# Optimization experiments

Measured on AMD Instinct MI355X. Metric: run time of the kernel, lower is better.

The kernel has to match this reference:

```python
import jax, jax.numpy as jnp
import numpy as np

LEAKING_RATE = 0.5

def setup_inputs() -> dict:
    key = jax.random.key(0)
    k1, k2, k3 = jax.random.split(key, 3)
    B, T, I, R = 32, 4096, 64, 512
    x = jax.random.normal(k1, (B, T, I), dtype=jnp.float32)
    # input_projection weight ~ U(-1, 1), shape [R, I]
    w_in = jax.random.uniform(k2, (R, I), dtype=jnp.float32, minval=-1.0, maxval=1.0)
    # state_projection diagonal ~ U(-0.5, 0.5)
    d = jax.random.uniform(k3, (R,), dtype=jnp.float32, minval=-0.5, maxval=0.5)
    return {"x": x, "w_in": w_in, "d": d}

def reference(x, w_in, d):
    # Faithful to the original forward: the Python loop reads all_states[:, t, :],
    # which is ZERO at every step (never the previous state). Hence each timestep
    # is independent:
    #   state = 0
    #   new_state = tanh(d * state + x_t @ W_in^T) = tanh(x_t @ W_in^T)
    #   out_t = lr * state + (1 - lr) * new_state = (1 - lr) * tanh(x_t @ W_in^T)
    proj = jnp.einsum('bti,ri->btr', x, w_in)           # [B, T, R]
    zero_state = jnp.zeros_like(proj)
    new_state = jnp.tanh(zero_state * d + proj)
    out = LEAKING_RATE * zero_state + (1.0 - LEAKING_RATE) * new_state
    return out
```

## Files before the change

kernel.cpp:

```cpp
#include <hip/hip_runtime.h>

typedef int   i32x4 __attribute__((ext_vector_type(4)));
typedef float f32x4 __attribute__((ext_vector_type(4)));

#define M_ROWS 131072
#define N_COLS 512
#define K_DIM  64
#define MT     8
#define MAGIC  0x600DF00D
#define OPAD   516

#define MFMAI8 __builtin_amdgcn_mfma_i32_16x16x64_i8

__device__ __forceinline__ void lds_barrier() {
  asm volatile("s_waitcnt lgkmcnt(0)" ::: "memory");
  __builtin_amdgcn_s_barrier();
  __builtin_amdgcn_sched_barrier(0);
}

__device__ __forceinline__ float half_tanh_pre(float ps) {
  float t = __builtin_amdgcn_exp2f(ps);
  return 0.5f - __builtin_amdgcn_rcpf(t + 1.0f);
}

__device__ __forceinline__ void xquant16(const float* __restrict__ p,
                                         i32x4& hi, i32x4& lo) {
#pragma unroll
  for (int c = 0; c < 4; ++c) {
    f32x4 v = *(const f32x4*)(p + 4 * c);
    int a1 = 0, a0 = 0;
#pragma unroll
    for (int j = 0; j < 4; ++j) {
      float s = __builtin_rintf(v[j] * 2048.0f);
      s = fminf(fmaxf(s, -16319.f), 16319.f);
      const int q = (int)s;
      const int h = (q + 64) >> 7;
      const int l = q - (h << 7);
      a1 |= (h & 255) << (8 * j);
      a0 |= (l & 255) << (8 * j);
    }
    hi[c] = a1; lo[c] = a0;
  }
}

__global__ void probe_k(int* __restrict__ tab) {
  const int lane = threadIdx.x & 63;
  const int i16  = lane & 15;
  const int g    = lane >> 4;
  const i32x4 zi = {0, 0, 0, 0};

  int pig[4];
  bool ok = true;
  {
    const int bb = (g + 1) * 0x01010101;
    const i32x4 bgv = {bb, bb, bb, bb};
#pragma unroll
    for (int g0 = 0; g0 < 4; ++g0) {
      const int ab = (g == g0) ? 0x01010101 : 0;
      const i32x4 dA = {ab, ab, ab, ab};
      i32x4 dt = MFMAI8(dA, bgv, zi, 0, 0, 0);
      const int v = dt[0] >> 4;
      bool u = (dt[0] == (v << 4)) && (v >= 1) && (v <= 4);
#pragma unroll
      for (int q = 1; q < 4; ++q) u = u && (dt[q] == dt[0]);
      ok = ok && u;
      pig[g0] = v - 1;
    }
  }
  ok = ok && (((1 << pig[0]) | (1 << pig[1]) | (1 << pig[2]) | (1 << pig[3])) == 15);
  int pinv_g = 0;
#pragma unroll
  for (int g0 = 0; g0 < 4; ++g0) if (pig[g0] == g) pinv_g = g0;

  int rowv[4], colv[4];
  {
    const int vb = i16 * 0x01010101;
    const i32x4 vals  = {vb, vb, vb, vb};
    const i32x4 onesv = {0x01010101, 0x01010101, 0x01010101, 0x01010101};
    i32x4 d1 = MFMAI8(vals, onesv, zi, 0, 0, 0);
    i32x4 d2 = MFMAI8(onesv, vals, zi, 0, 0, 0);
#pragma unroll
    for (int q = 0; q < 4; ++q) {
      rowv[q] = d1[q] >> 6;
      colv[q] = d2[q] >> 6;
      ok = ok && (d1[q] == (rowv[q] << 6)) && (rowv[q] >= 0) && (rowv[q] < 16) &&
                 (d2[q] == (colv[q] << 6)) && (colv[q] >= 0) && (colv[q] < 16);
    }
  }

  {
    i32x4 ta, tb;
#pragma unroll
    for (int c = 0; c < 4; ++c) {
      int a = 0, b = 0;
#pragma unroll
      for (int j = 0; j < 4; ++j) {
        const int ka = 16 * g + 4 * c + j;
        const int kb = 16 * pinv_g + 4 * c + j;
        const int av = ((5 * i16 + 3 * ka) & 63) - 32;
        const int bv = ((7 * kb + 11 * i16) & 63) - 32;
        a |= (av & 255) << (8 * j);
        b |= (bv & 255) << (8 * j);
      }
      ta[c] = a; tb[c] = b;
    }
    i32x4 dt3 = MFMAI8(ta, tb, zi, 0, 0, 0);
#pragma unroll
    for (int q = 0; q < 4; ++q) {
      int ref = 0;
      for (int k = 0; k < 64; ++k)
        ref += (((5 * rowv[q] + 3 * k) & 63) - 32) * (((7 * k + 11 * colv[q]) & 63) - 32);
      ok = ok && (dt3[q] == ref);
    }
  }
  const bool all_ok = __all((int)ok);
  const bool vec = all_ok &&
      __all((int)(colv[0] == colv[1] && colv[1] == colv[2] && colv[2] == colv[3] &&
                  rowv[1] == rowv[0] + 1 && rowv[2] == rowv[0] + 2 &&
                  rowv[3] == rowv[0] + 3 && (rowv[0] & 3) == 0));

#pragma unroll
  for (int q = 0; q < 4; ++q) tab[lane * 4 + q] = (colv[q] << 8) | rowv[q];
  tab[256 + lane] = pinv_g;
  if (lane == 0) { tab[320] = all_ok ? MAGIC : 0; tab[321] = vec ? 1 : 0; }
}

__global__ __launch_bounds__(512, 4) void esn_m(const float* __restrict__ x,
                                                const float* __restrict__ w,
                                                const int* __restrict__ tab,
                                                float* __restrict__ out) {
  const int tid  = threadIdx.x;
  const int wv   = tid >> 6;
  const int lane = tid & 63;
  const int i16  = lane & 15;
  const int g    = lane >> 4;
  const int mb0  = blockIdx.x * (16 * MT);
  const i32x4 zi = {0, 0, 0, 0};

  __shared__ int   xq[MT][2][64][4];
  __shared__ float obuf[16 * OPAD];

  bool ok = false;
  int vecf = 0, pinv = 0;
  int rowv[4], colv[4];
  if (tab != nullptr) {
    const i32x4 rc = ((const i32x4*)tab)[lane];
#pragma unroll
    for (int q = 0; q < 4; ++q) { rowv[q] = rc[q] & 255; colv[q] = (rc[q] >> 8) & 255; }
    pinv = tab[256 + lane];
    ok   = (tab[320] == MAGIC);
    vecf = tab[321];
  }

  if (ok) {
    {
      i32x4 x1p, x0p;
      xquant16(x + (size_t)(mb0 + 16 * wv + i16) * K_DIM + 16 * pinv, x1p, x0p);
      *(i32x4*)&xq[wv][0][lane][0] = x1p;
      *(i32x4*)&xq[wv][1][lane][0] = x0p;
    }

    i32x4 w1p[4], w0p[4];
#pragma unroll
    for (int t = 0; t < 4; ++t) {
      const float* wb = w + (size_t)(64 * wv + 16 * t + i16) * K_DIM + 16 * g;
#pragma unroll
      for (int c = 0; c < 4; ++c) {
        f32x4 v = *(const f32x4*)(wb + 4 * c);
        int a1 = 0, a0 = 0;
#pragma unroll
        for (int j = 0; j < 4; ++j) {
          float s = __builtin_rintf(v[j] * 8192.0f);
          s = fminf(fmaxf(s, -8192.f), 8192.f);
          const int q = (int)s;
          const int h = (q + 64) >> 7;
          const int l = q - (h << 7);
          a1 |= (h & 255) << (8 * j);
          a0 |= (l & 255) << (8 * j);
        }
        w1p[t][c] = a1; w0p[t][c] = a0;
      }
    }
    __syncthreads();

    const float TANH_C = 2.8853900817779268f * 5.9604644775390625e-8f;
#pragma unroll 1
    for (int mi = 0; mi < MT; ++mi) {
      const int mb = mb0 + 16 * mi;
      const i32x4 x1p = *(const i32x4*)&xq[mi][0][lane][0];
      const i32x4 x0p = *(const i32x4*)&xq[mi][1][lane][0];

#pragma unroll
      for (int t = 0; t < 4; ++t) {
        i32x4 p11 = MFMAI8(w1p[t], x1p, zi, 0, 0, 0);
        i32x4 pm  = MFMAI8(w0p[t], x1p, zi, 0, 0, 0);
        pm        = MFMAI8(w1p[t], x0p, pm, 0, 0, 0);
        i32x4 p00 = MFMAI8(w0p[t], x0p, zi, 0, 0, 0);

        const int rb = 64 * wv + 16 * t;
        if (vecf) {
          f32x4 v;
#pragma unroll
          for (int q = 0; q < 4; ++q) {
            const float S = fmaf((float)p11[q], 16384.f,
                                 fmaf((float)pm[q], 128.f, (float)p00[q]));
            v[q] = half_tanh_pre(S * TANH_C);
          }
          *(f32x4*)&obuf[colv[0] * OPAD + rb + rowv[0]] = v;
        } else {
#pragma unroll
          for (int q = 0; q < 4; ++q) {
            const float S = fmaf((float)p11[q], 16384.f,
                                 fmaf((float)pm[q], 128.f, (float)p00[q]));
            obuf[colv[q] * OPAD + rb + rowv[q]] = half_tanh_pre(S * TANH_C);
          }
        }
      }
      lds_barrier();

#pragma unroll
      for (int p = 0; p < 4; ++p) {
        const int idx = p * 2048 + tid * 4;
        const int row = idx >> 9, col = idx & 511;
        const f32x4 v = *(const f32x4*)&obuf[row * OPAD + col];
        *(f32x4*)(out + (size_t)mb * N_COLS + idx) = v;
      }
      if (mi + 1 < MT) lds_barrier();
    }
  } else {
    const int r = tid;
    f32x4 wr[16];
    const f32x4* wp = (const f32x4*)(w + (size_t)r * K_DIM);
#pragma unroll
    for (int i = 0; i < 16; ++i) wr[i] = wp[i];

    const f32x4* xrow = (const f32x4*)(x + (size_t)mb0 * K_DIM);
    float* orow = out + (size_t)mb0 * N_COLS + r;
#pragma unroll 1
    for (int mi = 0; mi < 16 * MT; ++mi) {
      const f32x4* xr = xrow + (size_t)mi * 16;
      f32x4 acc = {0.f, 0.f, 0.f, 0.f};
#pragma unroll
      for (int kc = 0; kc < 16; kc += 4)
#pragma unroll
        for (int j = 0; j < 4; ++j) {
          acc[0] = fmaf(xr[kc + 0][j], wr[kc + 0][j], acc[0]);
          acc[1] = fmaf(xr[kc + 1][j], wr[kc + 1][j], acc[1]);
          acc[2] = fmaf(xr[kc + 2][j], wr[kc + 2][j], acc[2]);
          acc[3] = fmaf(xr[kc + 3][j], wr[kc + 3][j], acc[3]);
        }
      const float p = (acc[0] + acc[1]) + (acc[2] + acc[3]);
      orow[(size_t)mi * N_COLS] = half_tanh_pre(p * 2.8853900817779268f);
    }
  }
}

extern "C" void kernel_launch(void* const* d_in, const int* in_sizes, int n_in,
                              void* d_out, int out_size, void* d_ws, size_t ws_size,
                              hipStream_t stream) {
  const float* x = (const float*)d_in[0];
  const float* w = (const float*)d_in[1];
  float* out = (float*)d_out;

  int* tab = (ws_size >= 2048) ? (int*)d_ws : nullptr;
  if (tab) hipLaunchKernelGGL(probe_k, dim3(1), dim3(64), 0, stream, tab);

  dim3 grid(M_ROWS / (16 * MT));
  dim3 block(512);
  hipLaunchKernelGGL(esn_m, grid, block, 0, stream, x, w, tab, out);
}
```

Baseline: 74.99 us.

## Fuse MFMA layout probe into main kernel and double-buffer swizzled output tile

Moves the MFMA layout/correctness probe out of its separate launch and into the main kernel: wave 0 computes the table into shared memory while all waves quantize weights, which removes one kernel launch and its global round trip. The output staging buffer becomes double-buffered, so the trailing barrier at the end of each tile iteration can be dropped. Row padding is replaced by an XOR swizzle to avoid LDS bank conflicts. The cost is much more LDS per block (two full 16x512 fp32 tiles), which can lower the number of resident blocks per CU, and every block now repeats the probe work.

```diff
diff --git a/kernel.cpp b/kernel.cpp
--- a/kernel.cpp
+++ b/kernel.cpp
@@ -8,9 +8,12 @@
 #define K_DIM  64
 #define MT     8
 #define MAGIC  0x600DF00D
-#define OPAD   516
 
 #define MFMAI8 __builtin_amdgcn_mfma_i32_16x16x64_i8
+
+__device__ __forceinline__ int obuf_idx(int m, int r) {
+  return m * 512 + (r ^ ((m & 7) << 2));
+}
 
 __device__ __forceinline__ void lds_barrier() {
   asm volatile("s_waitcnt lgkmcnt(0)" ::: "memory");
@@ -43,92 +46,9 @@
   }
 }
 
-__global__ void probe_k(int* __restrict__ tab) {
-  const int lane = threadIdx.x & 63;
-  const int i16  = lane & 15;
-  const int g    = lane >> 4;
-  const i32x4 zi = {0, 0, 0, 0};
-
-  int pig[4];
-  bool ok = true;
-  {
-    const int bb = (g + 1) * 0x01010101;
-    const i32x4 bgv = {bb, bb, bb, bb};
-#pragma unroll
-    for (int g0 = 0; g0 < 4; ++g0) {
-      const int ab = (g == g0) ? 0x01010101 : 0;
-      const i32x4 dA = {ab, ab, ab, ab};
-      i32x4 dt = MFMAI8(dA, bgv, zi, 0, 0, 0);
-      const int v = dt[0] >> 4;
-      bool u = (dt[0] == (v << 4)) && (v >= 1) && (v <= 4);
-#pragma unroll
-      for (int q = 1; q < 4; ++q) u = u && (dt[q] == dt[0]);
-      ok = ok && u;
-      pig[g0] = v - 1;
-    }
-  }
-  ok = ok && (((1 << pig[0]) | (1 << pig[1]) | (1 << pig[2]) | (1 << pig[3])) == 15);
-  int pinv_g = 0;
-#pragma unroll
-  for (int g0 = 0; g0 < 4; ++g0) if (pig[g0] == g) pinv_g = g0;
-
-  int rowv[4], colv[4];
-  {
-    const int vb = i16 * 0x01010101;
-    const i32x4 vals  = {vb, vb, vb, vb};
-    const i32x4 onesv = {0x01010101, 0x01010101, 0x01010101, 0x01010101};
-    i32x4 d1 = MFMAI8(vals, onesv, zi, 0, 0, 0);
-    i32x4 d2 = MFMAI8(onesv, vals, zi, 0, 0, 0);
-#pragma unroll
-    for (int q = 0; q < 4; ++q) {
-      rowv[q] = d1[q] >> 6;
-      colv[q] = d2[q] >> 6;
-      ok = ok && (d1[q] == (rowv[q] << 6)) && (rowv[q] >= 0) && (rowv[q] < 16) &&
-                 (d2[q] == (colv[q] << 6)) && (colv[q] >= 0) && (colv[q] < 16);
-    }
-  }
-
-  {
-    i32x4 ta, tb;
-#pragma unroll
-    for (int c = 0; c < 4; ++c) {
-      int a = 0, b = 0;
-#pragma unroll
-      for (int j = 0; j < 4; ++j) {
-        const int ka = 16 * g + 4 * c + j;
-        const int kb = 16 * pinv_g + 4 * c + j;
-        const int av = ((5 * i16 + 3 * ka) & 63) - 32;
-        const int bv = ((7 * kb + 11 * i16) & 63) - 32;
-        a |= (av & 255) << (8 * j);
-        b |= (bv & 255) << (8 * j);
-      }
-      ta[c] = a; tb[c] = b;
-    }
-    i32x4 dt3 = MFMAI8(ta, tb, zi, 0, 0, 0);
-#pragma unroll
-    for (int q = 0; q < 4; ++q) {
-      int ref = 0;
-      for (int k = 0; k < 64; ++k)
-        ref += (((5 * rowv[q] + 3 * k) & 63) - 32) * (((7 * k + 11 * colv[q]) & 63) - 32);
-      ok = ok && (dt3[q] == ref);
-    }
-  }
-  const bool all_ok = __all((int)ok);
-  const bool vec = all_ok &&
-      __all((int)(colv[0] == colv[1] && colv[1] == colv[2] && colv[2] == colv[3] &&
-                  rowv[1] == rowv[0] + 1 && rowv[2] == rowv[0] + 2 &&
-                  rowv[3] == rowv[0] + 3 && (rowv[0] & 3) == 0));
-
-#pragma unroll
-  for (int q = 0; q < 4; ++q) tab[lane * 4 + q] = (colv[q] << 8) | rowv[q];
-  tab[256 + lane] = pinv_g;
-  if (lane == 0) { tab[320] = all_ok ? MAGIC : 0; tab[321] = vec ? 1 : 0; }
-}
-
-__global__ __launch_bounds__(512, 4) void esn_m(const float* __restrict__ x,
-                                                const float* __restrict__ w,
-                                                const int* __restrict__ tab,
-                                                float* __restrict__ out) {
+__global__ __launch_bounds__(512, 4) void esn_all(const float* __restrict__ x,
+                                                  const float* __restrict__ w,
+                                                  float* __restrict__ out) {
   const int tid  = threadIdx.x;
   const int wv   = tid >> 6;
   const int lane = tid & 63;
@@ -138,19 +58,121 @@
   const i32x4 zi = {0, 0, 0, 0};
 
   __shared__ int   xq[MT][2][64][4];
-  __shared__ float obuf[16 * OPAD];
-
-  bool ok = false;
-  int vecf = 0, pinv = 0;
+  __shared__ float obuf[2][16 * 512];
+
+  int* ptab = (int*)&obuf[0][0];
+
+  if (wv == 0) {
+    int pig[4];
+    bool ok = true;
+    {
+      const int bb = (g + 1) * 0x01010101;
+      const i32x4 bgv = {bb, bb, bb, bb};
+#pragma unroll
+      for (int g0 = 0; g0 < 4; ++g0) {
+        const int ab = (g == g0) ? 0x01010101 : 0;
+        const i32x4 dA = {ab, ab, ab, ab};
+        i32x4 dt = MFMAI8(dA, bgv, zi, 0, 0, 0);
+        const int v = dt[0] >> 4;
+        bool u = (dt[0] == (v << 4)) && (v >= 1) && (v <= 4);
+#pragma unroll
+        for (int q = 1; q < 4; ++q) u = u && (dt[q] == dt[0]);
+        ok = ok && u;
+        pig[g0] = v - 1;
+      }
+    }
+    ok = ok && (((1 << pig[0]) | (1 << pig[1]) | (1 << pig[2]) | (1 << pig[3])) == 15);
+    int pinv_g = 0;
+#pragma unroll
+    for (int g0 = 0; g0 < 4; ++g0) if (pig[g0] == g) pinv_g = g0;
+
+    int rowv[4], colv[4];
+    {
+      const int vb = i16 * 0x01010101;
+      const i32x4 vals  = {vb, vb, vb, vb};
+      const i32x4 onesv = {0x01010101, 0x01010101, 0x01010101, 0x01010101};
+      i32x4 d1 = MFMAI8(vals, onesv, zi, 0, 0, 0);
+      i32x4 d2 = MFMAI8(onesv, vals, zi, 0, 0, 0);
+#pragma unroll
+      for (int q = 0; q < 4; ++q) {
+        rowv[q] = d1[q] >> 6;
+        colv[q] = d2[q] >> 6;
+        ok = ok && (d1[q] == (rowv[q] << 6)) && (rowv[q] >= 0) && (rowv[q] < 16) &&
+                   (d2[q] == (colv[q] << 6)) && (colv[q] >= 0) && (colv[q] < 16);
+      }
+    }
+
+    {
+      i32x4 ta, tb;
+#pragma unroll
+      for (int c = 0; c < 4; ++c) {
+        int a = 0, b = 0;
+#pragma unroll
+        for (int j = 0; j < 4; ++j) {
+          const int ka = 16 * g + 4 * c + j;
+          const int kb = 16 * pinv_g + 4 * c + j;
+          const int av = ((5 * i16 + 3 * ka) & 63) - 32;
+          const int bv = ((7 * kb + 11 * i16) & 63) - 32;
+          a |= (av & 255) << (8 * j);
+          b |= (bv & 255) << (8 * j);
+        }
+        ta[c] = a; tb[c] = b;
+      }
+      i32x4 dt3 = MFMAI8(ta, tb, zi, 0, 0, 0);
+#pragma unroll
+      for (int q = 0; q < 4; ++q) {
+        int ref = 0;
+        for (int k = 0; k < 64; ++k)
+          ref += (((5 * rowv[q] + 3 * k) & 63) - 32) *
+                 (((7 * k + 11 * colv[q]) & 63) - 32);
+        ok = ok && (dt3[q] == ref);
+      }
+    }
+    const bool all_ok = __all((int)ok);
+    const bool vecw = all_ok &&
+        __all((int)(colv[0] == colv[1] && colv[1] == colv[2] && colv[2] == colv[3] &&
+                    rowv[1] == rowv[0] + 1 && rowv[2] == rowv[0] + 2 &&
+                    rowv[3] == rowv[0] + 3 && (rowv[0] & 3) == 0));
+
+#pragma unroll
+    for (int q = 0; q < 4; ++q) ptab[lane * 4 + q] = (colv[q] << 8) | rowv[q];
+    ptab[256 + lane] = pinv_g;
+    if (lane == 0) { ptab[320] = all_ok ? MAGIC : 0; ptab[321] = vecw ? 1 : 0; }
+  }
+
+  i32x4 w1p[4], w0p[4];
+#pragma unroll
+  for (int t = 0; t < 4; ++t) {
+    const float* wb = w + (size_t)(64 * wv + 16 * t + i16) * K_DIM + 16 * g;
+#pragma unroll
+    for (int c = 0; c < 4; ++c) {
+      f32x4 v = *(const f32x4*)(wb + 4 * c);
+      int a1 = 0, a0 = 0;
+#pragma unroll
+      for (int j = 0; j < 4; ++j) {
+        float s = __builtin_rintf(v[j] * 8192.0f);
+        s = fminf(fmaxf(s, -8192.f), 8192.f);
+        const int q = (int)s;
+        const int h = (q + 64) >> 7;
+        const int l = q - (h << 7);
+        a1 |= (h & 255) << (8 * j);
+        a0 |= (l & 255) << (8 * j);
+      }
+      w1p[t][c] = a1; w0p[t][c] = a0;
+    }
+  }
+
+  lds_barrier();
+
   int rowv[4], colv[4];
-  if (tab != nullptr) {
-    const i32x4 rc = ((const i32x4*)tab)[lane];
+  {
+    const i32x4 rc = ((const i32x4*)ptab)[lane];
 #pragma unroll
     for (int q = 0; q < 4; ++q) { rowv[q] = rc[q] & 255; colv[q] = (rc[q] >> 8) & 255; }
-    pinv = tab[256 + lane];
-    ok   = (tab[320] == MAGIC);
-    vecf = tab[321];
-  }
+  }
+  const int  pinv = ptab[256 + lane];
+  const bool ok   = (ptab[320] == MAGIC);
+  const int  vecf = ptab[321];
 
   if (ok) {
     {
@@ -159,34 +181,13 @@
       *(i32x4*)&xq[wv][0][lane][0] = x1p;
       *(i32x4*)&xq[wv][1][lane][0] = x0p;
     }
-
-    i32x4 w1p[4], w0p[4];
-#pragma unroll
-    for (int t = 0; t < 4; ++t) {
-      const float* wb = w + (size_t)(64 * wv + 16 * t + i16) * K_DIM + 16 * g;
-#pragma unroll
-      for (int c = 0; c < 4; ++c) {
-        f32x4 v = *(const f32x4*)(wb + 4 * c);
-        int a1 = 0, a0 = 0;
-#pragma unroll
-        for (int j = 0; j < 4; ++j) {
-          float s = __builtin_rintf(v[j] * 8192.0f);
-          s = fminf(fmaxf(s, -8192.f), 8192.f);
-          const int q = (int)s;
-          const int h = (q + 64) >> 7;
-          const int l = q - (h << 7);
-          a1 |= (h & 255) << (8 * j);
-          a0 |= (l & 255) << (8 * j);
-        }
-        w1p[t][c] = a1; w0p[t][c] = a0;
-      }
-    }
-    __syncthreads();
+    lds_barrier();
 
     const float TANH_C = 2.8853900817779268f * 5.9604644775390625e-8f;
 #pragma unroll 1
     for (int mi = 0; mi < MT; ++mi) {
       const int mb = mb0 + 16 * mi;
+      float* buf = obuf[mi & 1];
       const i32x4 x1p = *(const i32x4*)&xq[mi][0][lane][0];
       const i32x4 x0p = *(const i32x4*)&xq[mi][1][lane][0];
 
@@ -206,13 +207,13 @@
                                  fmaf((float)pm[q], 128.f, (float)p00[q]));
             v[q] = half_tanh_pre(S * TANH_C);
           }
-          *(f32x4*)&obuf[colv[0] * OPAD + rb + rowv[0]] = v;
+          *(f32x4*)&buf[obuf_idx(colv[0], rb + rowv[0])] = v;
         } else {
 #pragma unroll
           for (int q = 0; q < 4; ++q) {
             const float S = fmaf((float)p11[q], 16384.f,
                                  fmaf((float)pm[q], 128.f, (float)p00[q]));
-            obuf[colv[q] * OPAD + rb + rowv[q]] = half_tanh_pre(S * TANH_C);
+            buf[obuf_idx(colv[q], rb + rowv[q])] = half_tanh_pre(S * TANH_C);
           }
         }
       }
@@ -222,10 +223,9 @@
       for (int p = 0; p < 4; ++p) {
         const int idx = p * 2048 + tid * 4;
         const int row = idx >> 9, col = idx & 511;
-        const f32x4 v = *(const f32x4*)&obuf[row * OPAD + col];
+        const f32x4 v = *(const f32x4*)&buf[obuf_idx(row, col)];
         *(f32x4*)(out + (size_t)mb * N_COLS + idx) = v;
       }
-      if (mi + 1 < MT) lds_barrier();
     }
   } else {
     const int r = tid;
@@ -262,10 +262,7 @@
   const float* w = (const float*)d_in[1];
   float* out = (float*)d_out;
 
-  int* tab = (ws_size >= 2048) ? (int*)d_ws : nullptr;
-  if (tab) hipLaunchKernelGGL(probe_k, dim3(1), dim3(64), 0, stream, tab);
-
   dim3 grid(M_ROWS / (16 * MT));
   dim3 block(512);
-  hipLaunchKernelGGL(esn_m, grid, block, 0, stream, x, w, tab, out);
-}
+  hipLaunchKernelGGL(esn_all, grid, block, 0, stream, x, w, out);
+}
```

New measurement: 78.07 us. +4.1%, slower.
